# Kernel optimization log

Hardware: AMD Instinct MI355X
Metric: run time of the kernel (lower is better)

## Reference

```python
import jax, jax.numpy as jnp
import numpy as np

IN_DIM = 256
HID = 512
PAT = 10
B = 512
BN_EPS = 1e-5


def setup_inputs() -> dict:
    key = jax.random.key(0)
    ks = jax.random.split(key, 16)
    s = 0.05
    return {
        "x": jax.random.normal(ks[0], (B, IN_DIM), jnp.float32),
        # pattern_detector params
        "W1": jax.random.normal(ks[1], (HID, IN_DIM), jnp.float32) * s,
        "b1": jax.random.normal(ks[2], (HID,), jnp.float32) * s,
        "bn_gamma": 1.0 + jax.random.normal(ks[3], (HID,), jnp.float32) * s,
        "bn_beta": jax.random.normal(ks[4], (HID,), jnp.float32) * s,
        "bn_mean": jax.random.normal(ks[5], (HID,), jnp.float32) * s,
        "bn_var": jnp.ones((HID,), jnp.float32),
        "W2": jax.random.normal(ks[6], (HID // 2, HID), jnp.float32) * s,
        "b2": jax.random.normal(ks[7], (HID // 2,), jnp.float32) * s,
        "W3": jax.random.normal(ks[8], (PAT, HID // 2), jnp.float32) * s,
        "b3": jax.random.normal(ks[9], (PAT,), jnp.float32) * s,
        # similarity_layer params; first Linear weight [HID, 2*IN_DIM] split into
        # the half acting on x_i (Ws1_a) and the half acting on x_j (Ws1_b)
        "Ws1_a": jax.random.normal(ks[10], (HID, IN_DIM), jnp.float32) * s,
        "Ws1_b": jax.random.normal(ks[11], (HID, IN_DIM), jnp.float32) * s,
        "bs1": jax.random.normal(ks[12], (HID,), jnp.float32) * s,
        "ws2": jax.random.normal(ks[13], (HID,), jnp.float32) * s,
        "bs2": jax.random.normal(ks[14], (), jnp.float32) * s,
    }


def reference(x, W1, b1, bn_gamma, bn_beta, bn_mean, bn_var, W2, b2, W3, b3,
              Ws1_a, Ws1_b, bs1, ws2, bs2):
    # --- pattern_detector MLP (eval mode: BN uses running stats, dropout off) ---
    h = x @ W1.T + b1                                    # [B, HID]
    h = bn_gamma * (h - bn_mean) * jax.lax.rsqrt(bn_var + BN_EPS) + bn_beta
    h = jax.nn.relu(h)
    h2 = jax.nn.relu(h @ W2.T + b2)                      # [B, HID//2]
    pattern_scores = h2 @ W3.T + b3                      # [B, PAT]
    pattern_probs = jax.nn.softmax(pattern_scores, axis=-1)

    # --- pairwise similarity: sim(i,j) = MLP(concat(x_i, x_j)) ---
    # Linear([x_i; x_j]) = x_i @ Ws1_a^T + x_j @ Ws1_b^T + bs1, so precompute
    # the two GEMMs and broadcast-add instead of materializing [B,B,2*IN_DIM].
    A = x @ Ws1_a.T                                      # [B, HID]
    C = x @ Ws1_b.T                                      # [B, HID]
    hid = jax.nn.relu(A[:, None, :] + C[None, :, :] + bs1)  # [B, B, HID]
    logits = hid @ ws2 + bs2                             # [B, B]
    sim_full = jax.nn.sigmoid(logits)
    # Original loops i<j only and mirrors, diagonal stays 0. Results are
    # detached (.item()) in torch, so stop_gradient for faithfulness.
    iu = jnp.triu(jnp.ones((x.shape[0], x.shape[0]), sim_full.dtype), k=1)
    S = sim_full * iu
    similarities = jax.lax.stop_gradient(S + S.T)

    return pattern_probs, pattern_scores, similarities
```

## Files before the change

kernel.cpp:

```cpp
#include <hip/hip_runtime.h>
#include <math.h>

#define BN_EPS 1e-5f

typedef _Float16 half2v __attribute__((ext_vector_type(2)));
typedef _Float16 half4v __attribute__((ext_vector_type(4)));
typedef _Float16 half8v __attribute__((ext_vector_type(8)));

__device__ __forceinline__ float fdot2(half2v a, half2v b, float c) {
    return __builtin_amdgcn_fdot2(a, b, c, false);
}
__device__ __forceinline__ half2v cvt2(float a, float b) {
    return __builtin_bit_cast(half2v, __builtin_amdgcn_cvt_pkrtz(a, b));
}

__global__ __launch_bounds__(256) void fused3_gemm(
    const float* __restrict__ x,
    const float* __restrict__ W1, const float* __restrict__ b1,
    const float* __restrict__ g, const float* __restrict__ be,
    const float* __restrict__ mu, const float* __restrict__ va,
    const float* __restrict__ Wa, const float* __restrict__ bs1,
    const float* __restrict__ Wb,
    _Float16* __restrict__ h16, _Float16* __restrict__ A16,
    _Float16* __restrict__ C16)
{
    __shared__ half2v As16[16][36];
    __shared__ half2v Bs16[16][72];

    const int t  = threadIdx.x;
    const int m0 = blockIdx.y * 32;
    const int n0 = blockIdx.x * 64;
    const int z  = blockIdx.z;
    const int tx = t & 15, ty = t >> 4;
    const int lrow = t >> 3;
    const int lk4  = (t & 7) << 2;
    const int k2b  = lk4 >> 1;

    const float* __restrict__ W = (z == 0) ? W1 : (z == 1 ? Wa : Wb);

    float acc[2][4] = {};

    for (int kc = 0; kc < 256; kc += 32) {
        const float4 av  = *(const float4*)&x[(m0 + lrow) * 256 + kc + lk4];
        const float4 bv0 = *(const float4*)&W[(n0 + lrow) * 256 + kc + lk4];
        const float4 bv1 = *(const float4*)&W[(n0 + lrow + 32) * 256 + kc + lk4];

        As16[k2b + 0][lrow] = cvt2(av.x, av.y);
        As16[k2b + 1][lrow] = cvt2(av.z, av.w);
        Bs16[k2b + 0][lrow] = cvt2(bv0.x, bv0.y);
        Bs16[k2b + 1][lrow] = cvt2(bv0.z, bv0.w);
        Bs16[k2b + 0][lrow + 32] = cvt2(bv1.x, bv1.y);
        Bs16[k2b + 1][lrow + 32] = cvt2(bv1.z, bv1.w);
        __syncthreads();

        #pragma unroll
        for (int k2 = 0; k2 < 16; ++k2) {
            const half4v a4 = *(const half4v*)&As16[k2][ty * 2];
            const half8v b8 = *(const half8v*)&Bs16[k2][tx * 4];
            const half2v a0 = __builtin_shufflevector(a4, a4, 0, 1);
            const half2v a1 = __builtin_shufflevector(a4, a4, 2, 3);
            const half2v b0 = __builtin_shufflevector(b8, b8, 0, 1);
            const half2v b1h = __builtin_shufflevector(b8, b8, 2, 3);
            const half2v b2h = __builtin_shufflevector(b8, b8, 4, 5);
            const half2v b3h = __builtin_shufflevector(b8, b8, 6, 7);
            acc[0][0] = fdot2(a0, b0, acc[0][0]);
            acc[0][1] = fdot2(a0, b1h, acc[0][1]);
            acc[0][2] = fdot2(a0, b2h, acc[0][2]);
            acc[0][3] = fdot2(a0, b3h, acc[0][3]);
            acc[1][0] = fdot2(a1, b0, acc[1][0]);
            acc[1][1] = fdot2(a1, b1h, acc[1][1]);
            acc[1][2] = fdot2(a1, b2h, acc[1][2]);
            acc[1][3] = fdot2(a1, b3h, acc[1][3]);
        }
        __syncthreads();
    }

    const int n = n0 + tx * 4;
    #pragma unroll
    for (int i = 0; i < 2; ++i) {
        const int m = m0 + ty * 2 + i;
        half4v o;
        if (z == 0) {
            #pragma unroll
            for (int j = 0; j < 4; ++j) {
                float zz = acc[i][j] + b1[n + j];
                zz = g[n + j] * (zz - mu[n + j]) * rsqrtf(va[n + j] + BN_EPS) + be[n + j];
                o[j] = (_Float16)fmaxf(zz, 0.f);
            }
            *(half4v*)&h16[m * 512 + n] = o;
        } else if (z == 1) {
            #pragma unroll
            for (int j = 0; j < 4; ++j) o[j] = (_Float16)(acc[i][j] + bs1[n + j]);
            *(half4v*)&A16[m * 512 + n] = o;
        } else {
            #pragma unroll
            for (int j = 0; j < 4; ++j) o[j] = (_Float16)acc[i][j];
            *(half4v*)&C16[m * 512 + n] = o;
        }
    }
}

__global__ __launch_bounds__(512) void gemm_h2_kernel(
    const _Float16* __restrict__ h16, const float* __restrict__ W2,
    const float* __restrict__ b2, float* __restrict__ h2o)
{
    __shared__ half2v As16[2][16][36];
    __shared__ half2v Bs16[2][16][72];
    __shared__ float Ps[32][68];

    const int t  = threadIdx.x;
    const int gk = t >> 8;
    const int tl = t & 255;
    const int m0 = blockIdx.y * 32;
    const int n0 = blockIdx.x * 64;
    const int tx = tl & 15, ty = tl >> 4;
    const int kb = gk << 8;

    float acc[2][4] = {};

    for (int kc = 0; kc < 256; kc += 32) {
        const int kk = kb + kc;
        if (tl < 128) {
            const int arow = tl >> 2;
            const int ak8  = (tl & 3) << 3;
            const float4 av = *(const float4*)&h16[(m0 + arow) * 512 + kk + ak8];
            const half2v* ap = (const half2v*)&av;
            const int k2 = ak8 >> 1;
            As16[gk][k2 + 0][arow] = ap[0];
            As16[gk][k2 + 1][arow] = ap[1];
            As16[gk][k2 + 2][arow] = ap[2];
            As16[gk][k2 + 3][arow] = ap[3];
        }
        {
            const int brow = tl >> 2;
            const int bk8  = (tl & 3) << 3;
            const float4 bv0 = *(const float4*)&W2[(n0 + brow) * 512 + kk + bk8];
            const float4 bv1 = *(const float4*)&W2[(n0 + brow) * 512 + kk + bk8 + 4];
            const int k2 = bk8 >> 1;
            Bs16[gk][k2 + 0][brow] = cvt2(bv0.x, bv0.y);
            Bs16[gk][k2 + 1][brow] = cvt2(bv0.z, bv0.w);
            Bs16[gk][k2 + 2][brow] = cvt2(bv1.x, bv1.y);
            Bs16[gk][k2 + 3][brow] = cvt2(bv1.z, bv1.w);
        }
        __syncthreads();

        #pragma unroll
        for (int k2 = 0; k2 < 16; ++k2) {
            const half4v a4 = *(const half4v*)&As16[gk][k2][ty * 2];
            const half8v b8 = *(const half8v*)&Bs16[gk][k2][tx * 4];
            const half2v a0 = __builtin_shufflevector(a4, a4, 0, 1);
            const half2v a1 = __builtin_shufflevector(a4, a4, 2, 3);
            const half2v b0 = __builtin_shufflevector(b8, b8, 0, 1);
            const half2v b1h = __builtin_shufflevector(b8, b8, 2, 3);
            const half2v b2h = __builtin_shufflevector(b8, b8, 4, 5);
            const half2v b3h = __builtin_shufflevector(b8, b8, 6, 7);
            acc[0][0] = fdot2(a0, b0, acc[0][0]);
            acc[0][1] = fdot2(a0, b1h, acc[0][1]);
            acc[0][2] = fdot2(a0, b2h, acc[0][2]);
            acc[0][3] = fdot2(a0, b3h, acc[0][3]);
            acc[1][0] = fdot2(a1, b0, acc[1][0]);
            acc[1][1] = fdot2(a1, b1h, acc[1][1]);
            acc[1][2] = fdot2(a1, b2h, acc[1][2]);
            acc[1][3] = fdot2(a1, b3h, acc[1][3]);
        }
        __syncthreads();
    }

    if (gk == 1) {
        #pragma unroll
        for (int i = 0; i < 2; ++i)
            #pragma unroll
            for (int j = 0; j < 4; ++j)
                Ps[ty * 2 + i][tx * 4 + j] = acc[i][j];
    }
    __syncthreads();
    if (gk == 0) {
        const int n = n0 + tx * 4;
        #pragma unroll
        for (int i = 0; i < 2; ++i) {
            const int m = m0 + ty * 2 + i;
            float4 o;
            o.x = fmaxf(acc[i][0] + Ps[ty * 2 + i][tx * 4 + 0] + b2[n + 0], 0.f);
            o.y = fmaxf(acc[i][1] + Ps[ty * 2 + i][tx * 4 + 1] + b2[n + 1], 0.f);
            o.z = fmaxf(acc[i][2] + Ps[ty * 2 + i][tx * 4 + 2] + b2[n + 2], 0.f);
            o.w = fmaxf(acc[i][3] + Ps[ty * 2 + i][tx * 4 + 3] + b2[n + 3], 0.f);
            *(float4*)&h2o[m * 256 + n] = o;
        }
    }
}

__global__ __launch_bounds__(256) void head_kernel(
    const float* __restrict__ h2, const float* __restrict__ W3,
    const float* __restrict__ b3, float* __restrict__ out)
{
    const int t = threadIdx.x;
    const int lane = t & 63;
    const int r = blockIdx.x * 4 + (t >> 6);

    float p[10];
    #pragma unroll
    for (int q = 0; q < 10; ++q) p[q] = 0.f;

    #pragma unroll
    for (int kk = 0; kk < 4; ++kk) {
        const int k = lane + kk * 64;
        const float hv = h2[r * 256 + k];
        #pragma unroll
        for (int q = 0; q < 10; ++q)
            p[q] = fmaf(hv, W3[q * 256 + k], p[q]);
    }
    #pragma unroll
    for (int q = 0; q < 10; ++q) {
        #pragma unroll
        for (int off = 32; off > 0; off >>= 1)
            p[q] += __shfl_down(p[q], off);
    }
    if (lane == 0) {
        float s[10], m = -1e30f;
        #pragma unroll
        for (int q = 0; q < 10; ++q) { s[q] = p[q] + b3[q]; m = fmaxf(m, s[q]); }
        float e[10], sum = 0.f;
        #pragma unroll
        for (int q = 0; q < 10; ++q) { e[q] = __expf(s[q] - m); sum += e[q]; }
        const float inv = 1.f / sum;
        #pragma unroll
        for (int q = 0; q < 10; ++q) {
            out[r * 10 + q] = e[q] * inv;
            out[5120 + r * 10 + q] = s[q];
        }
    }
}

#define SIMS 260
__global__ __launch_bounds__(512) void sim_kernel(
    const _Float16* __restrict__ A16, const _Float16* __restrict__ C16,
    const float* __restrict__ ws2, const float* __restrict__ bs2,
    float* __restrict__ S)
{
    __shared__ _Float16 Rs[2][32][SIMS];
    __shared__ _Float16 Qs[2][32][SIMS];
    __shared__ half2v wsh[256];
    __shared__ float Ps[32][33];
    __shared__ float Tt[32][33];

    const int t  = threadIdx.x;
    const int gk = t >> 8;
    const int tl = t & 255;
    const int r0 = blockIdx.y * 32;
    const int q0 = blockIdx.x * 32;
    const bool diag = (r0 == q0);
    const _Float16* RsSrc = (r0 <= q0) ? A16 : C16;
    const _Float16* QsSrc = (r0 <= q0) ? C16 : A16;
    const int kbase = gk << 8;

    if (t < 256) {
        half2v w;
        w.x = (_Float16)ws2[2 * t];
        w.y = (_Float16)ws2[2 * t + 1];
        wsh[t] = w;
    }

    #pragma unroll
    for (int i = 0; i < 4; ++i) {
        const int idx = tl + i * 256;
        const int row = idx >> 5;
        const int c8  = idx & 31;
        const float4 vr = *(const float4*)&RsSrc[(r0 + row) * 512 + kbase + c8 * 8];
        const float4 vq = *(const float4*)&QsSrc[(q0 + row) * 512 + kbase + c8 * 8];
        char* dr = (char*)&Rs[gk][row][0] + c8 * 16;
        ((float2*)dr)[0] = make_float2(vr.x, vr.y);
        ((float2*)dr)[1] = make_float2(vr.z, vr.w);
        char* dq = (char*)&Qs[gk][row][0] + c8 * 16;
        ((float2*)dq)[0] = make_float2(vq.x, vq.y);
        ((float2*)dq)[1] = make_float2(vq.z, vq.w);
    }
    __syncthreads();

    const int tx = tl & 15, ty = tl >> 4;
    const half2v* rp0 = (const half2v*)&Rs[gk][ty * 2][0];
    const half2v* rp1 = (const half2v*)&Rs[gk][ty * 2 + 1][0];
    const half2v* qp0 = (const half2v*)&Qs[gk][tx * 2][0];
    const half2v* qp1 = (const half2v*)&Qs[gk][tx * 2 + 1][0];
    const half2v* wp  = &wsh[gk * 128];
    const half2v z2 = {(_Float16)0, (_Float16)0};

    float a00 = 0.f, a01 = 0.f, a10 = 0.f, a11 = 0.f;
    #pragma unroll 16
    for (int k2 = 0; k2 < 128; ++k2) {
        const half2v r0v = rp0[k2], r1v = rp1[k2];
        const half2v q0v = qp0[k2], q1v = qp1[k2];
        const half2v w2 = wp[k2];
        a00 = fdot2(__builtin_elementwise_max(r0v + q0v, z2), w2, a00);
        a01 = fdot2(__builtin_elementwise_max(r0v + q1v, z2), w2, a01);
        a10 = fdot2(__builtin_elementwise_max(r1v + q0v, z2), w2, a10);
        a11 = fdot2(__builtin_elementwise_max(r1v + q1v, z2), w2, a11);
    }

    if (gk == 1) {
        Ps[ty * 2 + 0][tx * 2 + 0] = a00;
        Ps[ty * 2 + 0][tx * 2 + 1] = a01;
        Ps[ty * 2 + 1][tx * 2 + 0] = a10;
        Ps[ty * 2 + 1][tx * 2 + 1] = a11;
    }
    __syncthreads();

    if (gk == 0) {
        const float bsv = bs2[0];
        float v[2][2];
        v[0][0] = a00 + Ps[ty * 2 + 0][tx * 2 + 0];
        v[0][1] = a01 + Ps[ty * 2 + 0][tx * 2 + 1];
        v[1][0] = a10 + Ps[ty * 2 + 1][tx * 2 + 0];
        v[1][1] = a11 + Ps[ty * 2 + 1][tx * 2 + 1];
        #pragma unroll
        for (int di = 0; di < 2; ++di)
            #pragma unroll
            for (int dj = 0; dj < 2; ++dj)
                v[di][dj] = 1.f / (1.f + __expf(-(v[di][dj] + bsv)));
        if (!diag) {
            #pragma unroll
            for (int di = 0; di < 2; ++di)
                *(float2*)&S[(r0 + ty * 2 + di) * 512 + q0 + tx * 2] =
                    make_float2(v[di][0], v[di][1]);
        } else {
            #pragma unroll
            for (int di = 0; di < 2; ++di)
                #pragma unroll
                for (int dj = 0; dj < 2; ++dj)
                    Tt[ty * 2 + di][tx * 2 + dj] = v[di][dj];
        }
    }
    if (diag) {
        __syncthreads();
        if (gk == 0) {
            #pragma unroll
            for (int di = 0; di < 2; ++di)
                #pragma unroll
                for (int dj = 0; dj < 2; ++dj) {
                    const int rl = ty * 2 + di, ql = tx * 2 + dj;
                    const float o = rl < ql ? Tt[rl][ql] : (rl > ql ? Tt[ql][rl] : 0.f);
                    S[(r0 + rl) * 512 + q0 + ql] = o;
                }
        }
    }
}

extern "C" void kernel_launch(void* const* d_in, const int* in_sizes, int n_in,
                              void* d_out, int out_size, void* d_ws, size_t ws_size,
                              hipStream_t stream)
{
    const float* x   = (const float*)d_in[0];
    const float* W1  = (const float*)d_in[1];
    const float* b1  = (const float*)d_in[2];
    const float* g   = (const float*)d_in[3];
    const float* be  = (const float*)d_in[4];
    const float* mu  = (const float*)d_in[5];
    const float* va  = (const float*)d_in[6];
    const float* W2  = (const float*)d_in[7];
    const float* b2  = (const float*)d_in[8];
    const float* W3  = (const float*)d_in[9];
    const float* b3  = (const float*)d_in[10];
    const float* Wa  = (const float*)d_in[11];
    const float* Wb  = (const float*)d_in[12];
    const float* bs1 = (const float*)d_in[13];
    const float* ws2 = (const float*)d_in[14];
    const float* bs2 = (const float*)d_in[15];

    float* out = (float*)d_out;
    _Float16* h16 = (_Float16*)d_ws;
    float* h2 = (float*)(h16 + 512 * 512);
    _Float16* A16 = (_Float16*)(h2 + 512 * 256);
    _Float16* C16 = A16 + 512 * 512;

    fused3_gemm<<<dim3(8, 16, 3), 256, 0, stream>>>(x, W1, b1, g, be, mu, va,
                                                    Wa, bs1, Wb, h16, A16, C16);
    gemm_h2_kernel<<<dim3(4, 16), 512, 0, stream>>>(h16, W2, b2, h2);
    head_kernel<<<128, 256, 0, stream>>>(h2, W3, b3, out);
    sim_kernel<<<dim3(16, 16), 512, 0, stream>>>(A16, C16, ws2, bs2, out + 10240);
}
```

Baseline: 119.3 us.

## Use MFMA for fused first-layer GEMMs and merge head into sim kernel

Replaces the fdot2-based first GEMM (x times W1/Wa/Wb) with MFMA 16x16x32 f16 instructions. It loads the full K=256 slabs of x and W into LDS once instead of looping over K chunks, and precomputes the BN scale and offset per column. It also folds the head/softmax kernel into the similarity kernel as extra blocks, saving one launch. The costs are larger LDS use, strided 2-byte output stores, and divergent block roles inside one kernel.

```diff
diff --git a/kernel.cpp b/kernel.cpp
--- a/kernel.cpp
+++ b/kernel.cpp
@@ -6,6 +6,8 @@
 typedef _Float16 half2v __attribute__((ext_vector_type(2)));
 typedef _Float16 half4v __attribute__((ext_vector_type(4)));
 typedef _Float16 half8v __attribute__((ext_vector_type(8)));
+typedef __fp16 fp16x8 __attribute__((ext_vector_type(8)));
+typedef float floatx4 __attribute__((ext_vector_type(4)));
 
 __device__ __forceinline__ float fdot2(half2v a, half2v b, float c) {
     return __builtin_amdgcn_fdot2(a, b, c, false);
@@ -13,8 +15,12 @@
 __device__ __forceinline__ half2v cvt2(float a, float b) {
     return __builtin_bit_cast(half2v, __builtin_amdgcn_cvt_pkrtz(a, b));
 }
-
-__global__ __launch_bounds__(256) void fused3_gemm(
+__device__ __forceinline__ floatx4 mfma16(half8v a, half8v b, floatx4 c) {
+    return __builtin_amdgcn_mfma_f32_16x16x32_f16(
+        __builtin_bit_cast(fp16x8, a), __builtin_bit_cast(fp16x8, b), c, 0, 0, 0);
+}
+
+__global__ __launch_bounds__(256) void fused3_mfma(
     const float* __restrict__ x,
     const float* __restrict__ W1, const float* __restrict__ b1,
     const float* __restrict__ g, const float* __restrict__ be,
@@ -24,78 +30,75 @@
     _Float16* __restrict__ h16, _Float16* __restrict__ A16,
     _Float16* __restrict__ C16)
 {
-    __shared__ half2v As16[16][36];
-    __shared__ half2v Bs16[16][72];
+    __shared__ _Float16 Xs[64][264];
+    __shared__ _Float16 Ws[32][264];
 
     const int t  = threadIdx.x;
-    const int m0 = blockIdx.y * 32;
-    const int n0 = blockIdx.x * 64;
+    const int n0 = blockIdx.x * 32;
+    const int m0 = blockIdx.y * 64;
     const int z  = blockIdx.z;
-    const int tx = t & 15, ty = t >> 4;
-    const int lrow = t >> 3;
-    const int lk4  = (t & 7) << 2;
-    const int k2b  = lk4 >> 1;
-
-    const float* __restrict__ W = (z == 0) ? W1 : (z == 1 ? Wa : Wb);
-
-    float acc[2][4] = {};
-
+    const float* __restrict__ Wp = (z == 0) ? W1 : (z == 1 ? Wa : Wb);
+
+    #pragma unroll
+    for (int i = 0; i < 16; ++i) {
+        const int cidx = t + i * 256;
+        const int row = cidx >> 6;
+        const int c4  = cidx & 63;
+        const float4 v = *(const float4*)&x[(m0 + row) * 256 + c4 * 4];
+        *(half2v*)&Xs[row][c4 * 4 + 0] = cvt2(v.x, v.y);
+        *(half2v*)&Xs[row][c4 * 4 + 2] = cvt2(v.z, v.w);
+    }
+    #pragma unroll
+    for (int i = 0; i < 8; ++i) {
+        const int cidx = t + i * 256;
+        const int row = cidx >> 6;
+        const int c4  = cidx & 63;
+        const float4 v = *(const float4*)&Wp[(n0 + row) * 256 + c4 * 4];
+        *(half2v*)&Ws[row][c4 * 4 + 0] = cvt2(v.x, v.y);
+        *(half2v*)&Ws[row][c4 * 4 + 2] = cvt2(v.z, v.w);
+    }
+    __syncthreads();
+
+    const int wave = t >> 6;
+    const int lane = t & 63;
+    const int wy = wave >> 1, wx = wave & 1;
+    const int lrow = lane & 15;
+    const int quad = lane >> 4;
+    const int kq = quad * 8;
+
+    floatx4 acc[2] = {{0.f, 0.f, 0.f, 0.f}, {0.f, 0.f, 0.f, 0.f}};
+
+    #pragma unroll
     for (int kc = 0; kc < 256; kc += 32) {
-        const float4 av  = *(const float4*)&x[(m0 + lrow) * 256 + kc + lk4];
-        const float4 bv0 = *(const float4*)&W[(n0 + lrow) * 256 + kc + lk4];
-        const float4 bv1 = *(const float4*)&W[(n0 + lrow + 32) * 256 + kc + lk4];
-
-        As16[k2b + 0][lrow] = cvt2(av.x, av.y);
-        As16[k2b + 1][lrow] = cvt2(av.z, av.w);
-        Bs16[k2b + 0][lrow] = cvt2(bv0.x, bv0.y);
-        Bs16[k2b + 1][lrow] = cvt2(bv0.z, bv0.w);
-        Bs16[k2b + 0][lrow + 32] = cvt2(bv1.x, bv1.y);
-        Bs16[k2b + 1][lrow + 32] = cvt2(bv1.z, bv1.w);
-        __syncthreads();
-
-        #pragma unroll
-        for (int k2 = 0; k2 < 16; ++k2) {
-            const half4v a4 = *(const half4v*)&As16[k2][ty * 2];
-            const half8v b8 = *(const half8v*)&Bs16[k2][tx * 4];
-            const half2v a0 = __builtin_shufflevector(a4, a4, 0, 1);
-            const half2v a1 = __builtin_shufflevector(a4, a4, 2, 3);
-            const half2v b0 = __builtin_shufflevector(b8, b8, 0, 1);
-            const half2v b1h = __builtin_shufflevector(b8, b8, 2, 3);
-            const half2v b2h = __builtin_shufflevector(b8, b8, 4, 5);
-            const half2v b3h = __builtin_shufflevector(b8, b8, 6, 7);
-            acc[0][0] = fdot2(a0, b0, acc[0][0]);
-            acc[0][1] = fdot2(a0, b1h, acc[0][1]);
-            acc[0][2] = fdot2(a0, b2h, acc[0][2]);
-            acc[0][3] = fdot2(a0, b3h, acc[0][3]);
-            acc[1][0] = fdot2(a1, b0, acc[1][0]);
-            acc[1][1] = fdot2(a1, b1h, acc[1][1]);
-            acc[1][2] = fdot2(a1, b2h, acc[1][2]);
-            acc[1][3] = fdot2(a1, b3h, acc[1][3]);
-        }
-        __syncthreads();
-    }
-
-    const int n = n0 + tx * 4;
-    #pragma unroll
-    for (int i = 0; i < 2; ++i) {
-        const int m = m0 + ty * 2 + i;
-        half4v o;
-        if (z == 0) {
-            #pragma unroll
-            for (int j = 0; j < 4; ++j) {
-                float zz = acc[i][j] + b1[n + j];
-                zz = g[n + j] * (zz - mu[n + j]) * rsqrtf(va[n + j] + BN_EPS) + be[n + j];
-                o[j] = (_Float16)fmaxf(zz, 0.f);
-            }
-            *(half4v*)&h16[m * 512 + n] = o;
-        } else if (z == 1) {
-            #pragma unroll
-            for (int j = 0; j < 4; ++j) o[j] = (_Float16)(acc[i][j] + bs1[n + j]);
-            *(half4v*)&A16[m * 512 + n] = o;
-        } else {
-            #pragma unroll
-            for (int j = 0; j < 4; ++j) o[j] = (_Float16)acc[i][j];
-            *(half4v*)&C16[m * 512 + n] = o;
+        const half8v a0 = *(const half8v*)&Xs[wy * 32 + lrow][kc + kq];
+        const half8v a1 = *(const half8v*)&Xs[wy * 32 + 16 + lrow][kc + kq];
+        const half8v b0 = *(const half8v*)&Ws[wx * 16 + lrow][kc + kq];
+        acc[0] = mfma16(a0, b0, acc[0]);
+        acc[1] = mfma16(a1, b0, acc[1]);
+    }
+
+    const int n = n0 + wx * 16 + lrow;
+    float scale, off;
+    if (z == 0) {
+        const float s = g[n] * rsqrtf(va[n] + BN_EPS);
+        scale = s;
+        off = (b1[n] - mu[n]) * s + be[n];
+    } else if (z == 1) {
+        scale = 1.f;
+        off = bs1[n];
+    } else {
+        scale = 1.f;
+        off = 0.f;
+    }
+    _Float16* __restrict__ dst = (z == 0) ? h16 : (z == 1 ? A16 : C16);
+    #pragma unroll
+    for (int mi = 0; mi < 2; ++mi) {
+        #pragma unroll
+        for (int r = 0; r < 4; ++r) {
+            const int m = m0 + wy * 32 + mi * 16 + quad * 4 + r;
+            float v = acc[mi][r] * scale + off;
+            if (z == 0) v = fmaxf(v, 0.f);
+            dst[m * 512 + n] = (_Float16)v;
         }
     }
 }
@@ -189,53 +192,13 @@
     }
 }
 
-__global__ __launch_bounds__(256) void head_kernel(
+#define SIMS 260
+__global__ __launch_bounds__(512) void tail_kernel(
     const float* __restrict__ h2, const float* __restrict__ W3,
-    const float* __restrict__ b3, float* __restrict__ out)
-{
-    const int t = threadIdx.x;
-    const int lane = t & 63;
-    const int r = blockIdx.x * 4 + (t >> 6);
-
-    float p[10];
-    #pragma unroll
-    for (int q = 0; q < 10; ++q) p[q] = 0.f;
-
-    #pragma unroll
-    for (int kk = 0; kk < 4; ++kk) {
-        const int k = lane + kk * 64;
-        const float hv = h2[r * 256 + k];
-        #pragma unroll
-        for (int q = 0; q < 10; ++q)
-            p[q] = fmaf(hv, W3[q * 256 + k], p[q]);
-    }
-    #pragma unroll
-    for (int q = 0; q < 10; ++q) {
-        #pragma unroll
-        for (int off = 32; off > 0; off >>= 1)
-            p[q] += __shfl_down(p[q], off);
-    }
-    if (lane == 0) {
-        float s[10], m = -1e30f;
-        #pragma unroll
-        for (int q = 0; q < 10; ++q) { s[q] = p[q] + b3[q]; m = fmaxf(m, s[q]); }
-        float e[10], sum = 0.f;
-        #pragma unroll
-        for (int q = 0; q < 10; ++q) { e[q] = __expf(s[q] - m); sum += e[q]; }
-        const float inv = 1.f / sum;
-        #pragma unroll
-        for (int q = 0; q < 10; ++q) {
-            out[r * 10 + q] = e[q] * inv;
-            out[5120 + r * 10 + q] = s[q];
-        }
-    }
-}
-
-#define SIMS 260
-__global__ __launch_bounds__(512) void sim_kernel(
+    const float* __restrict__ b3,
     const _Float16* __restrict__ A16, const _Float16* __restrict__ C16,
     const float* __restrict__ ws2, const float* __restrict__ bs2,
-    float* __restrict__ S)
+    float* __restrict__ out)
 {
     __shared__ _Float16 Rs[2][32][SIMS];
     __shared__ _Float16 Qs[2][32][SIMS];
@@ -243,11 +206,52 @@
     __shared__ float Ps[32][33];
     __shared__ float Tt[32][33];
 
-    const int t  = threadIdx.x;
+    const int bid = blockIdx.x;
+    const int t   = threadIdx.x;
+
+    if (bid >= 256) {
+        const int lane = t & 63;
+        const int r = (bid - 256) * 8 + (t >> 6);
+
+        float p[10];
+        #pragma unroll
+        for (int q = 0; q < 10; ++q) p[q] = 0.f;
+        #pragma unroll
+        for (int kk = 0; kk < 4; ++kk) {
+            const int k = lane + kk * 64;
+            const float hv = h2[r * 256 + k];
+            #pragma unroll
+            for (int q = 0; q < 10; ++q)
+                p[q] = fmaf(hv, W3[q * 256 + k], p[q]);
+        }
+        #pragma unroll
+        for (int q = 0; q < 10; ++q) {
+            #pragma unroll
+            for (int off = 32; off > 0; off >>= 1)
+                p[q] += __shfl_down(p[q], off);
+        }
+        if (lane == 0) {
+            float s[10], m = -1e30f;
+            #pragma unroll
+            for (int q = 0; q < 10; ++q) { s[q] = p[q] + b3[q]; m = fmaxf(m, s[q]); }
+            float e[10], sum = 0.f;
+            #pragma unroll
+            for (int q = 0; q < 10; ++q) { e[q] = __expf(s[q] - m); sum += e[q]; }
+            const float inv = 1.f / sum;
+            #pragma unroll
+            for (int q = 0; q < 10; ++q) {
+                out[r * 10 + q] = e[q] * inv;
+                out[5120 + r * 10 + q] = s[q];
+            }
+        }
+        return;
+    }
+
+    float* __restrict__ S = out + 10240;
     const int gk = t >> 8;
     const int tl = t & 255;
-    const int r0 = blockIdx.y * 32;
-    const int q0 = blockIdx.x * 32;
+    const int r0 = (bid >> 4) * 32;
+    const int q0 = (bid & 15) * 32;
     const bool diag = (r0 == q0);
     const _Float16* RsSrc = (r0 <= q0) ? A16 : C16;
     const _Float16* QsSrc = (r0 <= q0) ? C16 : A16;
@@ -371,9 +375,8 @@
     _Float16* A16 = (_Float16*)(h2 + 512 * 256);
     _Float16* C16 = A16 + 512 * 512;
 
-    fused3_gemm<<<dim3(8, 16, 3), 256, 0, stream>>>(x, W1, b1, g, be, mu, va,
+    fused3_mfma<<<dim3(16, 8, 3), 256, 0, stream>>>(x, W1, b1, g, be, mu, va,
                                                     Wa, bs1, Wb, h16, A16, C16);
     gemm_h2_kernel<<<dim3(4, 16), 512, 0, stream>>>(h16, W2, b2, h2);
-    head_kernel<<<128, 256, 0, stream>>>(h2, W3, b3, out);
-    sim_kernel<<<dim3(16, 16), 512, 0, stream>>>(A16, C16, ws2, bs2, out + 10240);
-}
+    tail_kernel<<<320, 512, 0, stream>>>(h2, W3, b3, A16, C16, ws2, bs2, out);
+}
```

Measured after the change: 111.0 us. -6.9%, faster.
